# Kernel tuning notes

Measured on AMD Instinct MI355X. Metric: run time of the kernel, lower is better.

## Reference

```python
import jax, jax.numpy as jnp
import numpy as np

B, GS, IN_H, GCN_H, LIN_H = 65536, 7, 5, 144, 128


def _xavier(key, shape):
    fan_in, fan_out = shape[0], shape[1]
    limit = np.sqrt(6.0 / (fan_in + fan_out)).astype(np.float32)
    return jax.random.uniform(key, shape, jnp.float32, -limit, limit)


def setup_inputs() -> dict:
    key = jax.random.key(0)
    ks = jax.random.split(key, 12)
    operations = jax.random.normal(ks[0], (B, GS, IN_H), jnp.float32)
    adjacency = (jax.random.uniform(ks[1], (B, GS, GS)) < 0.3).astype(jnp.float32)
    num_vertices = jax.random.randint(ks[2], (B,), 1, 8).astype(jnp.float32)
    w1_0 = _xavier(ks[3], (IN_H, GCN_H))
    w2_0 = _xavier(ks[4], (IN_H, GCN_H))
    w1_1 = _xavier(ks[5], (GCN_H, GCN_H))
    w2_1 = _xavier(ks[6], (GCN_H, GCN_H))
    w1_2 = _xavier(ks[7], (GCN_H, GCN_H))
    w2_2 = _xavier(ks[8], (GCN_H, GCN_H))
    fc1_w = _xavier(ks[9], (LIN_H, GCN_H))  # torch Linear stores [out, in]
    fc2_w = _xavier(ks[10], (1, LIN_H))
    return {
        'operations': operations, 'adjacency': adjacency, 'num_vertices': num_vertices,
        'w1_0': w1_0, 'w2_0': w2_0, 'w1_1': w1_1, 'w2_1': w2_1,
        'w1_2': w1_2, 'w2_2': w2_2, 'fc1_w': fc1_w, 'fc2_w': fc2_w,
    }


def _row_normalize(adj):
    # divide each row by its sum (matches torch normalize_adj)
    return adj / adj.sum(axis=2, keepdims=True)


def reference(operations, adjacency, num_vertices,
              w1_0, w2_0, w1_1, w2_1, w1_2, w2_2, fc1_w, fc2_w):
    gs = adjacency.shape[1]
    eye = jnp.eye(gs, dtype=adjacency.dtype)
    adj_d = _row_normalize(adjacency + eye)  # [B, gs, gs]
    x = operations
    for w1, w2 in ((w1_0, w2_0), (w1_1, w2_1), (w1_2, w2_2)):
        norm_adj = _row_normalize(adj_d)                      # identity in value, kept faithful
        inv_norm_adj = _row_normalize(adj_d.transpose(0, 2, 1))
        o1 = jax.nn.relu(jnp.einsum('bij,bjk->bik', norm_adj, x @ w1))
        o2 = jax.nn.relu(jnp.einsum('bij,bjk->bik', inv_norm_adj, x @ w2))
        x = (o1 + o2) * 0.5  # dropout is identity at inference
    pooled = x.sum(axis=1) / num_vertices[:, None]            # [B, gcn_hidden]
    h = pooled @ fc1_w.T                                      # [B, linear_hidden]
    out = (h @ fc2_w.T).reshape(-1)                           # [B]
    return out
```

## Files before the change

### kernel.cpp

```cpp
#include <hip/hip_runtime.h>


typedef _Float16 half8   __attribute__((ext_vector_type(8)));
typedef _Float16 half4_t __attribute__((ext_vector_type(4)));
typedef float    floatx16 __attribute__((ext_vector_type(16)));

constexpr int GS = 7;
constexpr int NI = 8;
constexpr int MROWS = NI * GS;
constexpr int H = 144;
constexpr int LSTRIDE = 2 * 5 * 9 * 512;
constexpr int WT_HALFS = 3 * LSTRIDE;
constexpr int FRAGS = 3 * 90 * 64;

static __device__ inline half8 bc(_Float16 v) {
    half8 h = {v, v, v, v, v, v, v, v};
    return h;
}

__global__ void prep_kernel(const float* __restrict__ w10, const float* __restrict__ w20,
                            const float* __restrict__ w11, const float* __restrict__ w21,
                            const float* __restrict__ w12, const float* __restrict__ w22,
                            const float* __restrict__ fc1, const float* __restrict__ fc2,
                            _Float16* __restrict__ wt, float* __restrict__ g)
{
    if (blockIdx.x == 68) {
        const int j = threadIdx.x;
        if (j < H) {
            float s = 0.f;
            for (int o = 0; o < 128; ++o) s = fmaf(fc2[o], fc1[o * H + j], s);
            g[j] = s;
        }
        return;
    }
    const int t = blockIdx.x * 256 + threadIdx.x;
    if (t >= FRAGS) return;
    const int l    = t / (90 * 64);
    const int r    = t - l * (90 * 64);
    const int frag = r >> 6;
    const int lane = r & 63;
    const int p    = frag / 45;
    const int rem  = frag - p * 45;
    const int nt   = rem / 9;
    const int ks   = rem - nt * 9;
    const int n    = nt * 32 + (lane & 31);
    const int k0   = ks * 16 + (lane >> 5) * 8;
    const float* W = (l == 0) ? (p ? w20 : w10)
                   : (l == 1) ? (p ? w21 : w11)
                              : (p ? w22 : w12);
    const int K = (l == 0) ? 5 : 144;
    half8 h = bc((_Float16)0);
    #pragma unroll
    for (int j = 0; j < 8; ++j) {
        const int k = k0 + j;
        if (n < H && k < K) h[j] = (_Float16)W[k * H + n];
    }
    *(half8*)(wt + (size_t)l * LSTRIDE + (size_t)frag * 512 + (size_t)lane * 8) = h;
}

template<int NK, int NT>
__device__ __forceinline__ void gemm_store(const _Float16* __restrict__ wl,
                                           const half8* bn, const half8* bi,
                                           const int lane, const int mrow,
                                           _Float16 (*sX)[152])
{
    const _Float16* a1p = wl + (size_t)(NT * 9) * 512 + (size_t)lane * 8;
    const _Float16* a2p = a1p + (size_t)(45 * 512);
    floatx16 acc1, acc2;
    #pragma unroll
    for (int i = 0; i < 16; ++i) { acc1[i] = 0.f; acc2[i] = 0.f; }
    #pragma unroll
    for (int ks = 0; ks < NK; ++ks) {
        const half8 a1 = *(const half8*)(a1p + (size_t)ks * 512);
        acc1 = __builtin_amdgcn_mfma_f32_32x32x16_f16(a1, bn[ks], acc1, 0, 0, 0);
        const half8 a2 = *(const half8*)(a2p + (size_t)ks * 512);
        acc2 = __builtin_amdgcn_mfma_f32_32x32x16_f16(a2, bi[ks], acc2, 0, 0, 0);
    }
    if (mrow < MROWS) {
        #pragma unroll
        for (int q = 0; q < 4; ++q) {
            if (NT < 4 || q < 2) {
                const int n0 = NT * 32 + 4 * (lane >> 5) + 8 * q;
                half4_t h;
                #pragma unroll
                for (int i = 0; i < 4; ++i) {
                    const float v1 = acc1[4 * q + i] > 0.f ? acc1[4 * q + i] : 0.f;
                    const float v2 = acc2[4 * q + i] > 0.f ? acc2[4 * q + i] : 0.f;
                    h[i] = (_Float16)(0.5f * (v1 + v2));
                }
                *(half4_t*)&sX[mrow][n0] = h;
            }
        }
    }
}

__global__ __launch_bounds__(256, 3)
void gcn_mfma(const float* __restrict__ ops, const float* __restrict__ adj,
              const float* __restrict__ nv,
              const _Float16* __restrict__ wt, const float* __restrict__ gw,
              float* __restrict__ out)
{
    __shared__ __align__(16) _Float16 sX [MROWS][152];
    __shared__ __align__(16) _Float16 sXn[MROWS][152];
    __shared__ __align__(16) _Float16 sXi[MROWS][152];
    __shared__ __align__(16) _Float16 sAh[NI][2][GS][8];

    float (*adjd)[GS][GS] = (float(*)[GS][GS])&sXn[0][0];

    const int tid  = threadIdx.x;
    const int lane = tid & 63;
    const int wv   = tid >> 6;
    const int ibase = blockIdx.x * NI;

    if (tid < MROWS) {
        const int item = tid / GS, r = tid % GS;
        const float* orow = ops + ((size_t)(ibase + item) * GS + r) * 5;
        half8 h = bc((_Float16)0);
        h[0] = (_Float16)orow[0]; h[1] = (_Float16)orow[1]; h[2] = (_Float16)orow[2];
        h[3] = (_Float16)orow[3]; h[4] = (_Float16)orow[4];
        *(half8*)&sX[tid][0] = h;
        *(half8*)&sX[tid][8] = bc((_Float16)0);

        const float* arow = adj + ((size_t)(ibase + item) * GS + r) * GS;
        float a[GS]; float s = 0.f;
        #pragma unroll
        for (int c = 0; c < GS; ++c) { a[c] = arow[c] + (c == r ? 1.f : 0.f); s += a[c]; }
        const float is = 1.f / s;
        #pragma unroll
        for (int c = 0; c < GS; ++c) {
            const float v = a[c] * is;
            adjd[item][r][c] = v;
            sAh[item][0][r][c] = (_Float16)v;
        }
        sAh[item][0][r][7] = (_Float16)0.f;
    }
    __syncthreads();
    if (tid < MROWS) {
        const int item = tid / GS, r = tid % GS;
        float v[GS]; float s = 0.f;
        #pragma unroll
        for (int k = 0; k < GS; ++k) { v[k] = adjd[item][k][r]; s += v[k]; }
        const float is = 1.f / s;
        #pragma unroll
        for (int k = 0; k < GS; ++k) sAh[item][1][r][k] = (_Float16)(v[k] * is);
        sAh[item][1][r][7] = (_Float16)0.f;
    }
    __syncthreads();

    const int mt     = wv & 1;
    const int arow31 = lane & 31;
    const int mrow   = mt * 32 + arow31;
    const int mrowc  = (mrow < MROWS) ? mrow : 0;
    const int khi    = (lane >> 5) * 8;

    {
        for (int u = tid; u < MROWS * 2; u += 256) {
            const int row = u >> 1, cb = u & 1;
            const int item = row / GS, rr = row - item * GS;
            const int c0 = cb * 8;
            const half8 aN = *(const half8*)&sAh[item][0][rr][0];
            const half8 aI = *(const half8*)&sAh[item][1][rr][0];
            half8 an = bc((_Float16)0), ai = bc((_Float16)0);
            #pragma unroll
            for (int j = 0; j < GS; ++j) {
                const half8 xj = *(const half8*)&sX[item * GS + j][c0];
                an += bc(aN[j]) * xj;
                ai += bc(aI[j]) * xj;
            }
            *(half8*)&sXn[row][c0] = an;
            *(half8*)&sXi[row][c0] = ai;
        }
        __syncthreads();

        half8 bn[1], bi[1];
        bn[0] = *(const half8*)&sXn[mrowc][khi];
        bi[0] = *(const half8*)&sXi[mrowc][khi];

        if (wv < 2) {
            gemm_store<1, 0>(wt, bn, bi, lane, mrow, sX);
            gemm_store<1, 1>(wt, bn, bi, lane, mrow, sX);
            gemm_store<1, 2>(wt, bn, bi, lane, mrow, sX);
        } else {
            gemm_store<1, 3>(wt, bn, bi, lane, mrow, sX);
            gemm_store<1, 4>(wt, bn, bi, lane, mrow, sX);
        }
        __syncthreads();
    }

    for (int layer = 1; layer < 3; ++layer) {
        const _Float16* wl = wt + (size_t)layer * LSTRIDE;

        for (int u = tid; u < MROWS * 18; u += 256) {
            const int row = u / 18, cb = u - row * 18;
            const int item = row / GS, rr = row - item * GS;
            const int c0 = cb * 8;
            const half8 aN = *(const half8*)&sAh[item][0][rr][0];
            const half8 aI = *(const half8*)&sAh[item][1][rr][0];
            half8 an = bc((_Float16)0), ai = bc((_Float16)0);
            #pragma unroll
            for (int j = 0; j < GS; ++j) {
                const half8 xj = *(const half8*)&sX[item * GS + j][c0];
                an += bc(aN[j]) * xj;
                ai += bc(aI[j]) * xj;
            }
            *(half8*)&sXn[row][c0] = an;
            *(half8*)&sXi[row][c0] = ai;
        }
        __syncthreads();

        half8 bn[9], bi[9];
        #pragma unroll
        for (int ks = 0; ks < 9; ++ks) {
            bn[ks] = *(const half8*)&sXn[mrowc][ks * 16 + khi];
            bi[ks] = *(const half8*)&sXi[mrowc][ks * 16 + khi];
        }

        if (wv < 2) {
            gemm_store<9, 0>(wl, bn, bi, lane, mrow, sX);
            gemm_store<9, 1>(wl, bn, bi, lane, mrow, sX);
            gemm_store<9, 2>(wl, bn, bi, lane, mrow, sX);
        } else {
            gemm_store<9, 3>(wl, bn, bi, lane, mrow, sX);
            gemm_store<9, 4>(wl, bn, bi, lane, mrow, sX);
        }
        __syncthreads();
    }

    if (tid < NI * 16) {
        const int item = tid >> 4, part = tid & 15;
        float s = 0.f;
        #pragma unroll
        for (int c = 0; c < 9; ++c) {
            const int j = part * 9 + c;
            const float gj = gw[j];
            #pragma unroll
            for (int i = 0; i < GS; ++i)
                s = fmaf((float)sX[item * GS + i][j], gj, s);
        }
        s += __shfl_xor(s, 1);
        s += __shfl_xor(s, 2);
        s += __shfl_xor(s, 4);
        s += __shfl_xor(s, 8);
        if (part == 0) out[ibase + item] = s / nv[ibase + item];
    }
}

extern "C" void kernel_launch(void* const* d_in, const int* in_sizes, int n_in,
                              void* d_out, int out_size, void* d_ws, size_t ws_size,
                              hipStream_t stream) {
    const float* ops = (const float*)d_in[0];
    const float* adj = (const float*)d_in[1];
    const float* nv  = (const float*)d_in[2];
    const float* w10 = (const float*)d_in[3];
    const float* w20 = (const float*)d_in[4];
    const float* w11 = (const float*)d_in[5];
    const float* w21 = (const float*)d_in[6];
    const float* w12 = (const float*)d_in[7];
    const float* w22 = (const float*)d_in[8];
    const float* fc1 = (const float*)d_in[9];
    const float* fc2 = (const float*)d_in[10];

    _Float16* wt = (_Float16*)d_ws;
    float*    g  = (float*)((char*)d_ws + (size_t)WT_HALFS * 2);

    prep_kernel<<<69, 256, 0, stream>>>(w10, w20, w11, w21, w12, w22,
                                        fc1, fc2, wt, g);
    gcn_mfma<<<65536 / NI, 256, 0, stream>>>(ops, adj, nv, wt, g, (float*)d_out);
}
```

Baseline: 270.9 us.

## Reassign MFMA work so each wave reuses weight fragments across both row tiles

Reorganizes the per-layer GEMM so each wave owns one 32-column N tile and computes both 32-row M tiles, loading each weight fragment once and applying it to two B operands. Waves 2 and 3 also split the fifth N tile by M half. Previously, waves 0-1 and 2-3 each loaded every weight fragment redundantly for their own M tile. The aim is to halve global weight fragment loads and balance MFMA counts across waves, at the cost of more live accumulator registers (six floatx16), which may pressure occupancy under launch_bounds(256,3).

```diff
diff --git a/kernel.cpp b/kernel.cpp
--- a/kernel.cpp
+++ b/kernel.cpp
@@ -58,40 +58,101 @@
     *(half8*)(wt + (size_t)l * LSTRIDE + (size_t)frag * 512 + (size_t)lane * 8) = h;
 }
 
-template<int NK, int NT>
-__device__ __forceinline__ void gemm_store(const _Float16* __restrict__ wl,
-                                           const half8* bn, const half8* bi,
-                                           const int lane, const int mrow,
-                                           _Float16 (*sX)[152])
+template<int NK, int CB>
+static __device__ __forceinline__ void layer_pass(const _Float16* __restrict__ wl,
+                                                  const int tid, const int lane, const int wv,
+                                                  _Float16 (*sX)[152],
+                                                  _Float16 (*sXn)[152], _Float16 (*sXi)[152],
+                                                  const _Float16 (*sAh)[2][GS][8])
 {
-    const _Float16* a1p = wl + (size_t)(NT * 9) * 512 + (size_t)lane * 8;
-    const _Float16* a2p = a1p + (size_t)(45 * 512);
-    floatx16 acc1, acc2;
-    #pragma unroll
-    for (int i = 0; i < 16; ++i) { acc1[i] = 0.f; acc2[i] = 0.f; }
+    for (int u = tid; u < MROWS * CB; u += 256) {
+        const int row = u / CB, cb = u - row * CB;
+        const int item = row / GS, rr = row - item * GS;
+        const int c0 = cb * 8;
+        const half8 aN = *(const half8*)&sAh[item][0][rr][0];
+        const half8 aI = *(const half8*)&sAh[item][1][rr][0];
+        half8 an = bc((_Float16)0), ai = bc((_Float16)0);
+        #pragma unroll
+        for (int j = 0; j < GS; ++j) {
+            const half8 xj = *(const half8*)&sX[item * GS + j][c0];
+            an += bc(aN[j]) * xj;
+            ai += bc(aI[j]) * xj;
+        }
+        *(half8*)&sXn[row][c0] = an;
+        *(half8*)&sXi[row][c0] = ai;
+    }
+    __syncthreads();
+
+    const int  nt    = wv;
+    const bool extra = (wv >= 2);
+    const int  em    = wv & 1;
+    const int  khi   = (lane >> 5) * 8;
+    const int  r0    = lane & 31;
+    const int  r1    = 32 + r0;
+    const int  r1c   = (r1 < MROWS) ? r1 : (MROWS - 1);
+
+    floatx16 a1m0, a1m1, a2m0, a2m1, e1, e2;
+    #pragma unroll
+    for (int i = 0; i < 16; ++i) {
+        a1m0[i] = 0.f; a1m1[i] = 0.f; a2m0[i] = 0.f; a2m1[i] = 0.f;
+        e1[i] = 0.f; e2[i] = 0.f;
+    }
+
     #pragma unroll
     for (int ks = 0; ks < NK; ++ks) {
-        const half8 a1 = *(const half8*)(a1p + (size_t)ks * 512);
-        acc1 = __builtin_amdgcn_mfma_f32_32x32x16_f16(a1, bn[ks], acc1, 0, 0, 0);
-        const half8 a2 = *(const half8*)(a2p + (size_t)ks * 512);
-        acc2 = __builtin_amdgcn_mfma_f32_32x32x16_f16(a2, bi[ks], acc2, 0, 0, 0);
-    }
-    if (mrow < MROWS) {
-        #pragma unroll
-        for (int q = 0; q < 4; ++q) {
-            if (NT < 4 || q < 2) {
-                const int n0 = NT * 32 + 4 * (lane >> 5) + 8 * q;
-                half4_t h;
-                #pragma unroll
-                for (int i = 0; i < 4; ++i) {
-                    const float v1 = acc1[4 * q + i] > 0.f ? acc1[4 * q + i] : 0.f;
-                    const float v2 = acc2[4 * q + i] > 0.f ? acc2[4 * q + i] : 0.f;
-                    h[i] = (_Float16)(0.5f * (v1 + v2));
-                }
-                *(half4_t*)&sX[mrow][n0] = h;
+        const int c = ks * 16 + khi;
+        const half8 bn0 = *(const half8*)&sXn[r0][c];
+        const half8 bn1 = *(const half8*)&sXn[r1c][c];
+        const half8 bi0 = *(const half8*)&sXi[r0][c];
+        const half8 bi1 = *(const half8*)&sXi[r1c][c];
+        const _Float16* f1 = wl + (size_t)((nt * 9 + ks) * 512) + (size_t)lane * 8;
+        const half8 A1 = *(const half8*)f1;
+        const half8 A2 = *(const half8*)(f1 + 45 * 512);
+        a1m0 = __builtin_amdgcn_mfma_f32_32x32x16_f16(A1, bn0, a1m0, 0, 0, 0);
+        a1m1 = __builtin_amdgcn_mfma_f32_32x32x16_f16(A1, bn1, a1m1, 0, 0, 0);
+        a2m0 = __builtin_amdgcn_mfma_f32_32x32x16_f16(A2, bi0, a2m0, 0, 0, 0);
+        a2m1 = __builtin_amdgcn_mfma_f32_32x32x16_f16(A2, bi1, a2m1, 0, 0, 0);
+        if (extra) {
+            const _Float16* f4 = wl + (size_t)((36 + ks) * 512) + (size_t)lane * 8;
+            const half8 E1 = *(const half8*)f4;
+            const half8 E2 = *(const half8*)(f4 + 45 * 512);
+            e1 = __builtin_amdgcn_mfma_f32_32x32x16_f16(E1, em ? bn1 : bn0, e1, 0, 0, 0);
+            e2 = __builtin_amdgcn_mfma_f32_32x32x16_f16(E2, em ? bi1 : bi0, e2, 0, 0, 0);
+        }
+    }
+
+    #pragma unroll
+    for (int q = 0; q < 4; ++q) {
+        const int n0 = nt * 32 + 4 * (lane >> 5) + 8 * q;
+        half4_t h0, h1;
+        #pragma unroll
+        for (int i = 0; i < 4; ++i) {
+            float v1 = a1m0[4 * q + i]; v1 = v1 > 0.f ? v1 : 0.f;
+            float v2 = a2m0[4 * q + i]; v2 = v2 > 0.f ? v2 : 0.f;
+            h0[i] = (_Float16)(0.5f * (v1 + v2));
+            float w1 = a1m1[4 * q + i]; w1 = w1 > 0.f ? w1 : 0.f;
+            float w2 = a2m1[4 * q + i]; w2 = w2 > 0.f ? w2 : 0.f;
+            h1[i] = (_Float16)(0.5f * (w1 + w2));
+        }
+        *(half4_t*)&sX[r0][n0] = h0;
+        if (r0 < MROWS - 32) *(half4_t*)&sX[r1][n0] = h1;
+    }
+    if (extra) {
+        #pragma unroll
+        for (int q = 0; q < 2; ++q) {
+            const int n0 = 128 + 4 * (lane >> 5) + 8 * q;
+            half4_t h;
+            #pragma unroll
+            for (int i = 0; i < 4; ++i) {
+                float v1 = e1[4 * q + i]; v1 = v1 > 0.f ? v1 : 0.f;
+                float v2 = e2[4 * q + i]; v2 = v2 > 0.f ? v2 : 0.f;
+                h[i] = (_Float16)(0.5f * (v1 + v2));
             }
-        }
-    }
+            const int rr = em * 32 + r0;
+            if (rr < MROWS) *(half4_t*)&sX[rr][n0] = h;
+        }
+    }
+    __syncthreads();
 }
 
 __global__ __launch_bounds__(256, 3)
@@ -122,10 +183,10 @@
         *(half8*)&sX[tid][8] = bc((_Float16)0);
 
         const float* arow = adj + ((size_t)(ibase + item) * GS + r) * GS;
-        float a[GS]; float s = 0.f;
-        #pragma unroll
-        for (int c = 0; c < GS; ++c) { a[c] = arow[c] + (c == r ? 1.f : 0.f); s += a[c]; }
-        const float is = 1.f / s;
+        float a[GS]; float sm = 0.f;
+        #pragma unroll
+        for (int c = 0; c < GS; ++c) { a[c] = arow[c] + (c == r ? 1.f : 0.f); sm += a[c]; }
+        const float is = 1.f / sm;
         #pragma unroll
         for (int c = 0; c < GS; ++c) {
             const float v = a[c] * is;
@@ -137,94 +198,19 @@
     __syncthreads();
     if (tid < MROWS) {
         const int item = tid / GS, r = tid % GS;
-        float v[GS]; float s = 0.f;
-        #pragma unroll
-        for (int k = 0; k < GS; ++k) { v[k] = adjd[item][k][r]; s += v[k]; }
-        const float is = 1.f / s;
+        float v[GS]; float sm = 0.f;
+        #pragma unroll
+        for (int k = 0; k < GS; ++k) { v[k] = adjd[item][k][r]; sm += v[k]; }
+        const float is = 1.f / sm;
         #pragma unroll
         for (int k = 0; k < GS; ++k) sAh[item][1][r][k] = (_Float16)(v[k] * is);
         sAh[item][1][r][7] = (_Float16)0.f;
     }
     __syncthreads();
 
-    const int mt     = wv & 1;
-    const int arow31 = lane & 31;
-    const int mrow   = mt * 32 + arow31;
-    const int mrowc  = (mrow < MROWS) ? mrow : 0;
-    const int khi    = (lane >> 5) * 8;
-
-    {
-        for (int u = tid; u < MROWS * 2; u += 256) {
-            const int row = u >> 1, cb = u & 1;
-            const int item = row / GS, rr = row - item * GS;
-            const int c0 = cb * 8;
-            const half8 aN = *(const half8*)&sAh[item][0][rr][0];
-            const half8 aI = *(const half8*)&sAh[item][1][rr][0];
-            half8 an = bc((_Float16)0), ai = bc((_Float16)0);
-            #pragma unroll
-            for (int j = 0; j < GS; ++j) {
-                const half8 xj = *(const half8*)&sX[item * GS + j][c0];
-                an += bc(aN[j]) * xj;
-                ai += bc(aI[j]) * xj;
-            }
-            *(half8*)&sXn[row][c0] = an;
-            *(half8*)&sXi[row][c0] = ai;
-        }
-        __syncthreads();
-
-        half8 bn[1], bi[1];
-        bn[0] = *(const half8*)&sXn[mrowc][khi];
-        bi[0] = *(const half8*)&sXi[mrowc][khi];
-
-        if (wv < 2) {
-            gemm_store<1, 0>(wt, bn, bi, lane, mrow, sX);
-            gemm_store<1, 1>(wt, bn, bi, lane, mrow, sX);
-            gemm_store<1, 2>(wt, bn, bi, lane, mrow, sX);
-        } else {
-            gemm_store<1, 3>(wt, bn, bi, lane, mrow, sX);
-            gemm_store<1, 4>(wt, bn, bi, lane, mrow, sX);
-        }
-        __syncthreads();
-    }
-
-    for (int layer = 1; layer < 3; ++layer) {
-        const _Float16* wl = wt + (size_t)layer * LSTRIDE;
-
-        for (int u = tid; u < MROWS * 18; u += 256) {
-            const int row = u / 18, cb = u - row * 18;
-            const int item = row / GS, rr = row - item * GS;
-            const int c0 = cb * 8;
-            const half8 aN = *(const half8*)&sAh[item][0][rr][0];
-            const half8 aI = *(const half8*)&sAh[item][1][rr][0];
-            half8 an = bc((_Float16)0), ai = bc((_Float16)0);
-            #pragma unroll
-            for (int j = 0; j < GS; ++j) {
-                const half8 xj = *(const half8*)&sX[item * GS + j][c0];
-                an += bc(aN[j]) * xj;
-                ai += bc(aI[j]) * xj;
-            }
-            *(half8*)&sXn[row][c0] = an;
-            *(half8*)&sXi[row][c0] = ai;
-        }
-        __syncthreads();
-
-        half8 bn[9], bi[9];
-        #pragma unroll
-        for (int ks = 0; ks < 9; ++ks) {
-            bn[ks] = *(const half8*)&sXn[mrowc][ks * 16 + khi];
-            bi[ks] = *(const half8*)&sXi[mrowc][ks * 16 + khi];
-        }
-
-        if (wv < 2) {
-            gemm_store<9, 0>(wl, bn, bi, lane, mrow, sX);
-            gemm_store<9, 1>(wl, bn, bi, lane, mrow, sX);
-            gemm_store<9, 2>(wl, bn, bi, lane, mrow, sX);
-        } else {
-            gemm_store<9, 3>(wl, bn, bi, lane, mrow, sX);
-            gemm_store<9, 4>(wl, bn, bi, lane, mrow, sX);
-        }
-        __syncthreads();
-    }
+    layer_pass<1, 2>(wt,                        tid, lane, wv, sX, sXn, sXi, sAh);
+    layer_pass<9, 18>(wt + (size_t)1 * LSTRIDE, tid, lane, wv, sX, sXn, sXi, sAh);
+    layer_pass<9, 18>(wt + (size_t)2 * LSTRIDE, tid, lane, wv, sX, sXn, sXi, sAh);
 
     if (tid < NI * 16) {
         const int item = tid >> 4, part = tid & 15;
```

Measured after the change: 268.8 us. Within noise of the previous version (-0.8%).
